# Performance work log

Measured on AMD Instinct MI355X. Metric: run time of the kernel, lower is better.

Reference implementation:

```python
import jax, jax.numpy as jnp
import numpy as np
import math

IN_CH, OUT_CH, RANK, MODES, HEAD, BATCH = 64, 64, 8, 8192, 4, 32


def setup_inputs() -> dict:
    key = jax.random.key(0)
    kx, k1, k2, k3 = jax.random.split(key, 4)
    scale = 1.0 / math.sqrt(IN_CH * OUT_CH)
    x = jax.random.normal(kx, (BATCH, IN_CH, MODES), dtype=jnp.float32)
    # Note: in the torch module, self.U1 has in_channels rows and is used as the
    # FIRST contraction ('irkh'), while self.U2 has out_channels rows and is the
    # LAST ('oskh') — the jit'd function's arg names are swapped relative to the
    # module attributes. We name params by their role here.
    U_in = scale * jax.random.uniform(k1, (IN_CH, RANK, MODES, HEAD), dtype=jnp.float32)   # self.U1
    M = scale * jax.random.uniform(k2, (RANK, RANK, MODES, HEAD), dtype=jnp.float32)       # self.M
    U_out = scale * jax.random.uniform(k3, (OUT_CH, RANK, MODES, HEAD), dtype=jnp.float32) # self.U2
    return {"x": x, "U_in": U_in, "M": M, "U_out": U_out}


def reference(x, U_in, M, U_out):
    # x: [b, i, k] -> r: [b, r, k, h]
    r = jnp.einsum('irkh,bik->brkh', U_in, x)
    # mix ranks per (mode, head): [b, s, k, h]
    s = jnp.einsum('rskh,brkh->bskh', M, r)
    # project to out channels, sum over heads: [b, o, k]
    out = jnp.einsum('oskh,bskh->bok', U_out, s)
    return out
```

## Files before the change

### kernel.cpp

```cpp
#include <hip/hip_runtime.h>


static constexpr int IN_CH  = 64;
static constexpr int OUT_CH = 64;
static constexpr int RANK   = 8;
static constexpr int MODES  = 8192;
static constexpr int KT     = 16;
static constexpr int CROWS  = 64;
static constexpr int CF4    = CROWS * KT;

typedef const __attribute__((address_space(1))) void* gas_t;
typedef __attribute__((address_space(3))) void* las_t;

__device__ __forceinline__ void fma_s4(float4& a, const float4 w, const float v) {
    a.x = fmaf(w.x, v, a.x); a.y = fmaf(w.y, v, a.y);
    a.z = fmaf(w.z, v, a.z); a.w = fmaf(w.w, v, a.w);
}
__device__ __forceinline__ void fma_44(float4& a, const float4 w, const float4 v) {
    a.x = fmaf(w.x, v.x, a.x); a.y = fmaf(w.y, v.y, a.y);
    a.z = fmaf(w.z, v.z, a.z); a.w = fmaf(w.w, v.w, a.w);
}

__device__ __forceinline__ void stage_chunk(const float4* gbase, float4* lbuf,
                                            int wid, int lane) {
    const int sub = lane >> 4;
    const int col = lane & 15;
#pragma unroll
    for (int j = 0; j < 4; ++j) {
        const int row0 = wid * 16 + j * 4;
        const float4* src = gbase + (size_t)(row0 + sub) * MODES + col;
        float4* dst = lbuf + row0 * KT;
        __builtin_amdgcn_global_load_lds((gas_t)src, (las_t)dst, 16, 0, 0);
    }
}

__global__ __launch_bounds__(256, 4) void diag_lr_fused(
    const float*  __restrict__ x,
    const float4* __restrict__ Uin,
    const float4* __restrict__ Mw,
    const float4* __restrict__ Uout,
    float*        __restrict__ out)
{
    __shared__ float4 lds[2][CF4];

    const int t    = threadIdx.x;
    const int kk   = t & 15;
    const int brow = t >> 4;
    const int lane = t & 63;
    const int wid  = t >> 6;
    const int bid  = blockIdx.x;
    const int ktile = bid & 511;
    const int b     = ((bid >> 9) << 4) | brow;
    const int k0    = ktile * KT;
    const int k     = k0 + kk;

    const float4* UinB = Uin  + k0;
    const float4* MB   = Mw   + k0;
    const float4* UoB  = Uout + k0;
    const float*  xp   = x   + (size_t)b * (IN_CH  * MODES) + k;
    float*        op   = out + (size_t)b * (OUT_CH * MODES) + k;

    stage_chunk(UinB, &lds[0][0], wid, lane);
    float xc[8];
#pragma unroll
    for (int ii = 0; ii < 8; ++ii) xc[ii] = xp[ii * MODES];

    float4 racc[RANK];
#pragma unroll
    for (int r = 0; r < RANK; ++r) racc[r] = make_float4(0.f, 0.f, 0.f, 0.f);

#pragma unroll
    for (int c = 0; c < 8; ++c) {
        const int buf = c & 1;
        const float4* nxt = (c < 7) ? (UinB + (size_t)(c + 1) * CROWS * MODES) : MB;
        stage_chunk(nxt, &lds[buf ^ 1][0], wid, lane);
        asm volatile("s_waitcnt vmcnt(4)" ::: "memory");
        __builtin_amdgcn_s_barrier();
        asm volatile("" ::: "memory");
        float xn[8];
        if (c < 7) {
#pragma unroll
            for (int ii = 0; ii < 8; ++ii) xn[ii] = xp[((c + 1) * 8 + ii) * MODES];
        }
        const float4* Lb = &lds[buf][0];
#pragma unroll
        for (int ii = 0; ii < 8; ++ii)
#pragma unroll
            for (int r = 0; r < RANK; ++r)
                fma_s4(racc[r], Lb[(ii * 8 + r) * KT + kk], xc[ii]);
        asm volatile("" ::: "memory");
        __builtin_amdgcn_s_barrier();
        if (c < 7) {
#pragma unroll
            for (int ii = 0; ii < 8; ++ii) xc[ii] = xn[ii];
        }
    }

    float4 sacc[RANK];
#pragma unroll
    for (int s = 0; s < RANK; ++s) sacc[s] = make_float4(0.f, 0.f, 0.f, 0.f);
    {
        stage_chunk(UoB, &lds[1][0], wid, lane);
        asm volatile("s_waitcnt vmcnt(4)" ::: "memory");
        __builtin_amdgcn_s_barrier();
        asm volatile("" ::: "memory");
        const float4* Lb = &lds[0][0];
#pragma unroll
        for (int r = 0; r < RANK; ++r)
#pragma unroll
            for (int s = 0; s < RANK; ++s)
                fma_44(sacc[s], Lb[(r * 8 + s) * KT + kk], racc[r]);
        asm volatile("" ::: "memory");
        __builtin_amdgcn_s_barrier();
    }

#pragma unroll
    for (int c = 0; c < 8; ++c) {
        const int buf = (c + 1) & 1;
        if (c < 7) {
            stage_chunk(UoB + (size_t)(c + 1) * CROWS * MODES, &lds[buf ^ 1][0], wid, lane);
            asm volatile("s_waitcnt vmcnt(4)" ::: "memory");
        } else {
            asm volatile("s_waitcnt vmcnt(0)" ::: "memory");
        }
        __builtin_amdgcn_s_barrier();
        asm volatile("" ::: "memory");
        const float4* Lb = &lds[buf][0];
#pragma unroll
        for (int oo = 0; oo < 8; ++oo) {
            float4 a = make_float4(0.f, 0.f, 0.f, 0.f);
#pragma unroll
            for (int s = 0; s < RANK; ++s)
                fma_44(a, Lb[(oo * 8 + s) * KT + kk], sacc[s]);
            op[(c * 8 + oo) * MODES] = (a.x + a.y) + (a.z + a.w);
        }
        if (c < 7) {
            asm volatile("" ::: "memory");
            __builtin_amdgcn_s_barrier();
        }
    }
}

extern "C" void kernel_launch(void* const* d_in, const int* in_sizes, int n_in,
                              void* d_out, int out_size, void* d_ws, size_t ws_size,
                              hipStream_t stream) {
    const float*  x    = (const float*)d_in[0];
    const float4* Uin  = (const float4*)d_in[1];
    const float4* Mw   = (const float4*)d_in[2];
    const float4* Uout = (const float4*)d_in[3];
    float* out = (float*)d_out;

    dim3 grid(1024), block(256);
    hipLaunchKernelGGL(diag_lr_fused, grid, block, 0, stream, x, Uin, Mw, Uout, out);
}
```

Measured before the change: 78.95 us.

## Process two batch rows per thread to halve weight staging traffic

Each block now handles all 32 batches for one 16-mode k-tile, with every thread computing two batch rows that share each LDS weight read. The grid halves to 512 blocks, so the per-mode weights (U_in, M, U_out) are fetched from global memory once per tile instead of twice. The x loads for the next chunk are now issued before the barrier, with the vmcnt wait adjusted to match. The cost is doubled accumulator registers and a lower occupancy bound (launch_bounds 2), plus only 512 blocks to spread across the CUs.

After: 82.75 us. +4.8%, slower.

```diff
diff --git a/kernel.cpp b/kernel.cpp
--- a/kernel.cpp
+++ b/kernel.cpp
@@ -34,7 +34,7 @@
     }
 }
 
-__global__ __launch_bounds__(256, 4) void diag_lr_fused(
+__global__ __launch_bounds__(256, 2) void diag_lr_fused(
     const float*  __restrict__ x,
     const float4* __restrict__ Uin,
     const float4* __restrict__ Mw,
@@ -45,60 +45,73 @@
 
     const int t    = threadIdx.x;
     const int kk   = t & 15;
-    const int brow = t >> 4;
+    const int bs   = t >> 4;
     const int lane = t & 63;
     const int wid  = t >> 6;
-    const int bid  = blockIdx.x;
-    const int ktile = bid & 511;
-    const int b     = ((bid >> 9) << 4) | brow;
-    const int k0    = ktile * KT;
-    const int k     = k0 + kk;
+    const int k0   = blockIdx.x * KT;
+    const int k    = k0 + kk;
 
     const float4* UinB = Uin  + k0;
     const float4* MB   = Mw   + k0;
     const float4* UoB  = Uout + k0;
-    const float*  xp   = x   + (size_t)b * (IN_CH  * MODES) + k;
-    float*        op   = out + (size_t)b * (OUT_CH * MODES) + k;
+    const float*  xp0 = x + (size_t)bs        * (IN_CH * MODES) + k;
+    const float*  xp1 = x + (size_t)(bs + 16) * (IN_CH * MODES) + k;
+    float*        op0 = out + (size_t)bs        * (OUT_CH * MODES) + k;
+    float*        op1 = out + (size_t)(bs + 16) * (OUT_CH * MODES) + k;
 
     stage_chunk(UinB, &lds[0][0], wid, lane);
-    float xc[8];
+    float xa[2][2][8];
 #pragma unroll
-    for (int ii = 0; ii < 8; ++ii) xc[ii] = xp[ii * MODES];
+    for (int ii = 0; ii < 8; ++ii) {
+        xa[0][0][ii] = xp0[ii * MODES];
+        xa[0][1][ii] = xp1[ii * MODES];
+    }
 
-    float4 racc[RANK];
+    float4 r0[RANK], r1[RANK];
 #pragma unroll
-    for (int r = 0; r < RANK; ++r) racc[r] = make_float4(0.f, 0.f, 0.f, 0.f);
+    for (int r = 0; r < RANK; ++r) {
+        r0[r] = make_float4(0.f, 0.f, 0.f, 0.f);
+        r1[r] = make_float4(0.f, 0.f, 0.f, 0.f);
+    }
 
 #pragma unroll
     for (int c = 0; c < 8; ++c) {
         const int buf = c & 1;
         const float4* nxt = (c < 7) ? (UinB + (size_t)(c + 1) * CROWS * MODES) : MB;
         stage_chunk(nxt, &lds[buf ^ 1][0], wid, lane);
-        asm volatile("s_waitcnt vmcnt(4)" ::: "memory");
+        if (c < 7) {
+#pragma unroll
+            for (int ii = 0; ii < 8; ++ii) {
+                xa[buf ^ 1][0][ii] = xp0[((c + 1) * 8 + ii) * MODES];
+                xa[buf ^ 1][1][ii] = xp1[((c + 1) * 8 + ii) * MODES];
+            }
+        }
+        if (c < 7) asm volatile("s_waitcnt vmcnt(20)" ::: "memory");
+        else       asm volatile("s_waitcnt vmcnt(4)"  ::: "memory");
         __builtin_amdgcn_s_barrier();
         asm volatile("" ::: "memory");
-        float xn[8];
-        if (c < 7) {
-#pragma unroll
-            for (int ii = 0; ii < 8; ++ii) xn[ii] = xp[((c + 1) * 8 + ii) * MODES];
-        }
         const float4* Lb = &lds[buf][0];
 #pragma unroll
-        for (int ii = 0; ii < 8; ++ii)
+        for (int ii = 0; ii < 8; ++ii) {
+            const float xv0 = xa[buf][0][ii];
+            const float xv1 = xa[buf][1][ii];
 #pragma unroll
-            for (int r = 0; r < RANK; ++r)
-                fma_s4(racc[r], Lb[(ii * 8 + r) * KT + kk], xc[ii]);
+            for (int r = 0; r < RANK; ++r) {
+                const float4 w = Lb[(ii * 8 + r) * KT + kk];
+                fma_s4(r0[r], w, xv0);
+                fma_s4(r1[r], w, xv1);
+            }
+        }
         asm volatile("" ::: "memory");
         __builtin_amdgcn_s_barrier();
-        if (c < 7) {
-#pragma unroll
-            for (int ii = 0; ii < 8; ++ii) xc[ii] = xn[ii];
-        }
     }
 
-    float4 sacc[RANK];
+    float4 s0[RANK], s1[RANK];
 #pragma unroll
-    for (int s = 0; s < RANK; ++s) sacc[s] = make_float4(0.f, 0.f, 0.f, 0.f);
+    for (int s = 0; s < RANK; ++s) {
+        s0[s] = make_float4(0.f, 0.f, 0.f, 0.f);
+        s1[s] = make_float4(0.f, 0.f, 0.f, 0.f);
+    }
     {
         stage_chunk(UoB, &lds[1][0], wid, lane);
         asm volatile("s_waitcnt vmcnt(4)" ::: "memory");
@@ -108,8 +121,11 @@
 #pragma unroll
         for (int r = 0; r < RANK; ++r)
 #pragma unroll
-            for (int s = 0; s < RANK; ++s)
-                fma_44(sacc[s], Lb[(r * 8 + s) * KT + kk], racc[r]);
+            for (int s = 0; s < RANK; ++s) {
+                const float4 w = Lb[(r * 8 + s) * KT + kk];
+                fma_44(s0[s], w, r0[r]);
+                fma_44(s1[s], w, r1[r]);
+            }
         asm volatile("" ::: "memory");
         __builtin_amdgcn_s_barrier();
     }
@@ -128,11 +144,16 @@
         const float4* Lb = &lds[buf][0];
 #pragma unroll
         for (int oo = 0; oo < 8; ++oo) {
-            float4 a = make_float4(0.f, 0.f, 0.f, 0.f);
+            float4 a0 = make_float4(0.f, 0.f, 0.f, 0.f);
+            float4 a1 = make_float4(0.f, 0.f, 0.f, 0.f);
 #pragma unroll
-            for (int s = 0; s < RANK; ++s)
-                fma_44(a, Lb[(oo * 8 + s) * KT + kk], sacc[s]);
-            op[(c * 8 + oo) * MODES] = (a.x + a.y) + (a.z + a.w);
+            for (int s = 0; s < RANK; ++s) {
+                const float4 w = Lb[(oo * 8 + s) * KT + kk];
+                fma_44(a0, w, s0[s]);
+                fma_44(a1, w, s1[s]);
+            }
+            op0[(c * 8 + oo) * MODES] = (a0.x + a0.y) + (a0.z + a0.w);
+            op1[(c * 8 + oo) * MODES] = (a1.x + a1.y) + (a1.z + a1.w);
         }
         if (c < 7) {
             asm volatile("" ::: "memory");
@@ -150,6 +171,6 @@
     const float4* Uout = (const float4*)d_in[3];
     float* out = (float*)d_out;
 
-    dim3 grid(1024), block(256);
+    dim3 grid(512), block(256);
     hipLaunchKernelGGL(diag_lr_fused, grid, block, 0, stream, x, Uin, Mw, Uout, out);
 }
```

## Use 512-thread blocks covering all batches with a 4-deep LDS staging ring

Applied to the files above, without the earlier changes.

Each block now covers all 32 batch rows for one 16-mode tile, so every weight chunk is loaded from global memory once per tile instead of twice, and the grid shrinks to 512 blocks. Weight staging moves from a 2-buffer ping-pong to a 4-buffer ring that prefetches two chunks ahead. This removes one barrier per chunk and uses hand-tuned vmcnt waits that also account for the interleaved x loads and output stores. The cost is more LDS per block, fewer blocks for the GPU, and fragile waitcnt arithmetic.

Measured after the change: 74.07 us. -6.2%, faster.

```diff
diff --git a/kernel.cpp b/kernel.cpp
--- a/kernel.cpp
+++ b/kernel.cpp
@@ -12,6 +12,8 @@
 typedef const __attribute__((address_space(1))) void* gas_t;
 typedef __attribute__((address_space(3))) void* las_t;
 
+#define FENCE asm volatile("" ::: "memory")
+
 __device__ __forceinline__ void fma_s4(float4& a, const float4 w, const float v) {
     a.x = fmaf(w.x, v, a.x); a.y = fmaf(w.y, v, a.y);
     a.z = fmaf(w.z, v, a.z); a.w = fmaf(w.w, v, a.w);
@@ -21,49 +23,55 @@
     a.z = fmaf(w.z, v.z, a.z); a.w = fmaf(w.w, v.w, a.w);
 }
 
-__device__ __forceinline__ void stage_chunk(const float4* gbase, float4* lbuf,
-                                            int wid, int lane) {
+__device__ __forceinline__ void stage_chunk8(const float4* gbase, float4* lbuf,
+                                             int wid, int lane) {
     const int sub = lane >> 4;
     const int col = lane & 15;
 #pragma unroll
-    for (int j = 0; j < 4; ++j) {
-        const int row0 = wid * 16 + j * 4;
+    for (int j = 0; j < 2; ++j) {
+        const int row0 = wid * 8 + j * 4;
         const float4* src = gbase + (size_t)(row0 + sub) * MODES + col;
         float4* dst = lbuf + row0 * KT;
         __builtin_amdgcn_global_load_lds((gas_t)src, (las_t)dst, 16, 0, 0);
     }
 }
 
-__global__ __launch_bounds__(256, 4) void diag_lr_fused(
+__global__ __launch_bounds__(512, 4) void diag_lr_fused(
     const float*  __restrict__ x,
     const float4* __restrict__ Uin,
     const float4* __restrict__ Mw,
     const float4* __restrict__ Uout,
     float*        __restrict__ out)
 {
-    __shared__ float4 lds[2][CF4];
+    __shared__ float4 lds[4][CF4];
 
     const int t    = threadIdx.x;
     const int kk   = t & 15;
-    const int brow = t >> 4;
+    const int b    = t >> 4;
     const int lane = t & 63;
     const int wid  = t >> 6;
-    const int bid  = blockIdx.x;
-    const int ktile = bid & 511;
-    const int b     = ((bid >> 9) << 4) | brow;
-    const int k0    = ktile * KT;
-    const int k     = k0 + kk;
+    const int k0   = blockIdx.x * KT;
+    const int k    = k0 + kk;
 
     const float4* UinB = Uin  + k0;
     const float4* MB   = Mw   + k0;
     const float4* UoB  = Uout + k0;
-    const float*  xp   = x   + (size_t)b * (IN_CH  * MODES) + k;
-    float*        op   = out + (size_t)b * (OUT_CH * MODES) + k;
+    const float*  xp = x   + (size_t)b * (IN_CH  * MODES) + k;
+    float*        op = out + (size_t)b * (OUT_CH * MODES) + k;
 
-    stage_chunk(UinB, &lds[0][0], wid, lane);
-    float xc[8];
+#define CHUNK_PTR(cc) ((cc) < 8 ? (UinB + (size_t)(cc) * CROWS * MODES) \
+                     : (cc) == 8 ? MB \
+                     : (UoB + (size_t)((cc) - 9) * CROWS * MODES))
+
+    float xa[2][8];
+
+    stage_chunk8(CHUNK_PTR(0), &lds[0][0], wid, lane);
+    FENCE;
 #pragma unroll
-    for (int ii = 0; ii < 8; ++ii) xc[ii] = xp[ii * MODES];
+    for (int ii = 0; ii < 8; ++ii) xa[0][ii] = xp[ii * MODES];
+    FENCE;
+    stage_chunk8(CHUNK_PTR(1), &lds[1][0], wid, lane);
+    FENCE;
 
     float4 racc[RANK];
 #pragma unroll
@@ -71,74 +79,71 @@
 
 #pragma unroll
     for (int c = 0; c < 8; ++c) {
-        const int buf = c & 1;
-        const float4* nxt = (c < 7) ? (UinB + (size_t)(c + 1) * CROWS * MODES) : MB;
-        stage_chunk(nxt, &lds[buf ^ 1][0], wid, lane);
-        asm volatile("s_waitcnt vmcnt(4)" ::: "memory");
+        asm volatile("s_waitcnt vmcnt(2)" ::: "memory");
         __builtin_amdgcn_s_barrier();
-        asm volatile("" ::: "memory");
-        float xn[8];
+        FENCE;
         if (c < 7) {
 #pragma unroll
-            for (int ii = 0; ii < 8; ++ii) xn[ii] = xp[((c + 1) * 8 + ii) * MODES];
+            for (int ii = 0; ii < 8; ++ii)
+                xa[(c + 1) & 1][ii] = xp[((c + 1) * 8 + ii) * MODES];
+            FENCE;
         }
-        const float4* Lb = &lds[buf][0];
+        stage_chunk8(CHUNK_PTR(c + 2), &lds[(c + 2) & 3][0], wid, lane);
+        FENCE;
+        const float4* Lb = &lds[c & 3][0];
 #pragma unroll
-        for (int ii = 0; ii < 8; ++ii)
+        for (int ii = 0; ii < 8; ++ii) {
+            const float xv = xa[c & 1][ii];
 #pragma unroll
             for (int r = 0; r < RANK; ++r)
-                fma_s4(racc[r], Lb[(ii * 8 + r) * KT + kk], xc[ii]);
-        asm volatile("" ::: "memory");
-        __builtin_amdgcn_s_barrier();
-        if (c < 7) {
-#pragma unroll
-            for (int ii = 0; ii < 8; ++ii) xc[ii] = xn[ii];
+                fma_s4(racc[r], Lb[(ii * 8 + r) * KT + kk], xv);
         }
+        FENCE;
     }
 
     float4 sacc[RANK];
 #pragma unroll
     for (int s = 0; s < RANK; ++s) sacc[s] = make_float4(0.f, 0.f, 0.f, 0.f);
     {
-        stage_chunk(UoB, &lds[1][0], wid, lane);
-        asm volatile("s_waitcnt vmcnt(4)" ::: "memory");
+        asm volatile("s_waitcnt vmcnt(2)" ::: "memory");
         __builtin_amdgcn_s_barrier();
-        asm volatile("" ::: "memory");
-        const float4* Lb = &lds[0][0];
+        FENCE;
+        stage_chunk8(CHUNK_PTR(10), &lds[10 & 3][0], wid, lane);
+        FENCE;
+        const float4* Lb = &lds[8 & 3][0];
 #pragma unroll
         for (int r = 0; r < RANK; ++r)
 #pragma unroll
             for (int s = 0; s < RANK; ++s)
                 fma_44(sacc[s], Lb[(r * 8 + s) * KT + kk], racc[r]);
-        asm volatile("" ::: "memory");
-        __builtin_amdgcn_s_barrier();
+        FENCE;
     }
 
 #pragma unroll
-    for (int c = 0; c < 8; ++c) {
-        const int buf = (c + 1) & 1;
-        if (c < 7) {
-            stage_chunk(UoB + (size_t)(c + 1) * CROWS * MODES, &lds[buf ^ 1][0], wid, lane);
-            asm volatile("s_waitcnt vmcnt(4)" ::: "memory");
-        } else {
-            asm volatile("s_waitcnt vmcnt(0)" ::: "memory");
+    for (int c = 9; c < 17; ++c) {
+        if      (c == 9)  asm volatile("s_waitcnt vmcnt(2)"  ::: "memory");
+        else if (c == 10) asm volatile("s_waitcnt vmcnt(10)" ::: "memory");
+        else if (c == 16) asm volatile("s_waitcnt vmcnt(16)" ::: "memory");
+        else              asm volatile("s_waitcnt vmcnt(18)" ::: "memory");
+        __builtin_amdgcn_s_barrier();
+        FENCE;
+        if (c + 2 <= 16) {
+            stage_chunk8(CHUNK_PTR(c + 2), &lds[(c + 2) & 3][0], wid, lane);
+            FENCE;
         }
-        __builtin_amdgcn_s_barrier();
-        asm volatile("" ::: "memory");
-        const float4* Lb = &lds[buf][0];
+        const float4* Lb = &lds[c & 3][0];
+        const int oc = c - 9;
 #pragma unroll
         for (int oo = 0; oo < 8; ++oo) {
             float4 a = make_float4(0.f, 0.f, 0.f, 0.f);
 #pragma unroll
             for (int s = 0; s < RANK; ++s)
                 fma_44(a, Lb[(oo * 8 + s) * KT + kk], sacc[s]);
-            op[(c * 8 + oo) * MODES] = (a.x + a.y) + (a.z + a.w);
+            op[(oc * 8 + oo) * MODES] = (a.x + a.y) + (a.z + a.w);
         }
-        if (c < 7) {
-            asm volatile("" ::: "memory");
-            __builtin_amdgcn_s_barrier();
-        }
+        FENCE;
     }
+#undef CHUNK_PTR
 }
 
 extern "C" void kernel_launch(void* const* d_in, const int* in_sizes, int n_in,
@@ -150,6 +155,6 @@
     const float4* Uout = (const float4*)d_in[3];
     float* out = (float*)d_out;
 
-    dim3 grid(1024), block(256);
+    dim3 grid(512), block(512);
     hipLaunchKernelGGL(diag_lr_fused, grid, block, 0, stream, x, Uin, Mw, Uout, out);
 }
```
